# Kernel optimization log

Measured on AMD Instinct MI355X. Metric: run time of the kernel, lower is better.

The kernel has to match this reference:

```python
import jax, jax.numpy as jnp
import numpy as np

B, T, DM = 2, 512, 1024
H, DH = 16, 64          # n_heads, d_head = d_model // n_heads
D, R = 32, 4            # d_manifold, metric_net rank
TEMP_MIN = 0.5


def _rope_tables(t_len, d_head):
    inv_freq = 1.0 / (10000.0 ** (jnp.arange(0, d_head, 2, dtype=jnp.float32) / d_head))
    t = jnp.arange(t_len, dtype=jnp.float32)
    freqs = t[:, None] * inv_freq[None, :]          # [T, d_head//2]
    emb = jnp.concatenate([freqs, freqs], axis=-1)  # [T, d_head]
    return jnp.cos(emb), jnp.sin(emb)


def _apply_rope(x, cos, sin):
    # x: [B, H, T, d_head]
    half = x.shape[-1] // 2
    x1, x2 = x[..., :half], x[..., half:]
    c1 = cos[None, None, :, :half]
    s1 = sin[None, None, :, :half]
    return jnp.concatenate([x1 * c1 - x2 * s1, x1 * s1 + x2 * c1], axis=-1)


def setup_inputs() -> dict:
    key = jax.random.key(0)
    ks = jax.random.split(key, 9)
    s = 0.02
    return {
        "x": jax.random.normal(ks[0], (B, T, DM), dtype=jnp.float32),
        "Wq": s * jax.random.normal(ks[1], (DM, DM), dtype=jnp.float32),
        "Wk": s * jax.random.normal(ks[2], (DM, DM), dtype=jnp.float32),
        "Wv": s * jax.random.normal(ks[3], (DM, DM), dtype=jnp.float32),
        "Wo": s * jax.random.normal(ks[4], (DM, DM), dtype=jnp.float32),
        "Wqm": s * jax.random.normal(ks[5], (DH, D), dtype=jnp.float32),
        "Wkm": s * jax.random.normal(ks[6], (DH, D), dtype=jnp.float32),
        "Wmetric": s * jax.random.normal(ks[7], (D, D * R), dtype=jnp.float32),
        "temperature": jnp.asarray(1.0, dtype=jnp.float32),
    }


def reference(x, Wq, Wk, Wv, Wo, Wqm, Wkm, Wmetric, temperature):
    b, t, c = x.shape
    # projections -> [B, H, T, d_head]
    def split_heads(y):
        return y.reshape(b, t, H, DH).transpose(0, 2, 1, 3)
    q = split_heads(x @ Wq)
    k = split_heads(x @ Wk)
    v = split_heads(x @ Wv)

    cos, sin = _rope_tables(t, DH)
    q = _apply_rope(q, cos, sin)
    k = _apply_rope(k, cos, sin)

    # manifold coordinates in (0,1): [B, H, T, D]
    qm = jax.nn.sigmoid(jnp.einsum('bhtd,dm->bhtm', q, Wqm))
    km = jax.nn.sigmoid(jnp.einsum('bhtd,dm->bhtm', k, Wkm))

    # low-rank metric factor U(q): [B, H, T, D, R]
    U = jnp.einsum('bhtm,mn->bhtn', qm, Wmetric).reshape(b, H, t, D, R)

    # Euclidean part: ||q_i - k_j||^2 = |q|^2 + |k|^2 - 2 q.k  -> [B,H,T,T]
    q2 = jnp.sum(qm * qm, axis=-1)
    k2 = jnp.sum(km * km, axis=-1)
    qk = jnp.einsum('bhid,bhjd->bhij', qm, km)
    dist_euc = q2[..., :, None] + k2[..., None, :] - 2.0 * qk

    # low-rank part: ||U_i^T (q_i - k_j)||^2, factorized as U_i^T q_i - U_i^T k_j
    Uq = jnp.einsum('bhidr,bhid->bhir', U, qm)          # [B,H,T,R]
    Uk = jnp.einsum('bhidr,bhjd->bhijr', U, km)         # [B,H,T,T,R]
    dist_lr = jnp.sum((Uq[:, :, :, None, :] - Uk) ** 2, axis=-1)

    dist_sq = jnp.maximum(dist_euc + dist_lr, 0.0)

    temp = jnp.maximum(temperature, TEMP_MIN)
    attn = -dist_sq / temp

    causal = jnp.triu(jnp.ones((t, t), dtype=bool), k=1)
    attn = jnp.where(causal[None, None], -jnp.inf, attn)
    attn = jax.nn.softmax(attn, axis=-1)

    out = jnp.einsum('bhij,bhjd->bhid', attn, v)        # [B,H,T,d_head]
    out = out.transpose(0, 2, 1, 3).reshape(b, t, c)
    return out @ Wo
```

## Files before the change

kernel.cpp:

```cpp
#include <hip/hip_runtime.h>
#include <cmath>

constexpr int B_  = 2;
constexpr int T_  = 512;
constexpr int DM_ = 1024;
constexpr int H_  = 16;
constexpr int DH_ = 64;
constexpr int D_  = 32;
constexpr int R_  = 4;
constexpr int BH_ = B_ * H_;

typedef __bf16 bf16x8 __attribute__((ext_vector_type(8)));
typedef float  f32x4  __attribute__((ext_vector_type(4)));
typedef unsigned short u16x8 __attribute__((ext_vector_type(8)));

__device__ __forceinline__ unsigned short f2bf(float f) {
    unsigned u = __float_as_uint(f);
    return (unsigned short)((u + 0x7fffu + ((u >> 16) & 1u)) >> 16);
}
__device__ __forceinline__ float bf2f(unsigned short v) {
    return __uint_as_float((unsigned)v << 16);
}
__device__ __forceinline__ void gload16(const void* g, void* l) {
    __builtin_amdgcn_global_load_lds(
        (const __attribute__((address_space(1))) void*)g,
        (__attribute__((address_space(3))) void*)l, 16, 0, 0);
}

__global__ __launch_bounds__(256) void prep_kernel(
    const float* __restrict__ x,
    const float* __restrict__ Wq, const float* __restrict__ Wk,
    const float* __restrict__ Wv, const float* __restrict__ Wo,
    unsigned short* __restrict__ xb,
    unsigned short* __restrict__ wqb, unsigned short* __restrict__ wkb,
    unsigned short* __restrict__ wvb, unsigned short* __restrict__ wob)
{
    const int t = threadIdx.x;
    const int z = blockIdx.z;
    if (z == 4) {
        int base = (blockIdx.y * 16 + blockIdx.x) * 4096 + t * 16;
#pragma unroll
        for (int c = 0; c < 4; ++c) {
            float4 v = *(const float4*)&x[base + c * 4];
            ushort4 o = { f2bf(v.x), f2bf(v.y), f2bf(v.z), f2bf(v.w) };
            *(ushort4*)&xb[base + c * 4] = o;
        }
        return;
    }
    __shared__ __align__(16) unsigned short Ls[64][72];
    const float* W = (z == 0) ? Wq : (z == 1) ? Wk : (z == 2) ? Wv : Wo;
    unsigned short* O = (z == 0) ? wqb : (z == 1) ? wkb : (z == 2) ? wvb : wob;
    const int k0 = blockIdx.x * 64;
    const int n0 = blockIdx.y * 64;
#pragma unroll
    for (int it = 0; it < 4; ++it) {
        int r = it * 16 + (t >> 4);
        int c = (t & 15) * 4;
        float4 v4 = *(const float4*)&W[(size_t)(k0 + r) * DM_ + n0 + c];
        Ls[c + 0][r] = f2bf(v4.x); Ls[c + 1][r] = f2bf(v4.y);
        Ls[c + 2][r] = f2bf(v4.z); Ls[c + 3][r] = f2bf(v4.w);
    }
    __syncthreads();
#pragma unroll
    for (int it = 0; it < 2; ++it) {
        int nl = it * 32 + (t >> 3);
        int kc = (t & 7) * 8;
        *(u16x8*)&O[(size_t)(n0 + nl) * DM_ + k0 + kc] = *(const u16x8*)&Ls[nl][kc];
    }
}

__global__ __launch_bounds__(256) void qkv_feat_gemm(
    const unsigned short* __restrict__ A,
    const unsigned short* __restrict__ wqb, const unsigned short* __restrict__ wkb,
    const unsigned short* __restrict__ wvb,
    const float* __restrict__ Wqm, const float* __restrict__ Wkm,
    const float* __restrict__ Wmetric,
    unsigned short* __restrict__ a_hi, unsigned short* __restrict__ a_lo,
    unsigned short* __restrict__ km_hi, unsigned short* __restrict__ km_lo,
    float* __restrict__ q2p, float* __restrict__ k2,
    unsigned short* __restrict__ Urb, unsigned short* __restrict__ vT)
{
    __shared__ union {
        struct { __align__(16) unsigned short As[64 * 64];
                 __align__(16) unsigned short Bs[64 * 64]; } g;
        struct { float Ct[64][65];
                 float qms[4][32]; float Us[4][128]; float Uqs[4][4]; } f;
    } sh;

    const int tid  = threadIdx.x;
    const int lane = tid & 63;
    const int w    = tid >> 6;
    const int wm   = (w & 1) * 32;
    const int wn   = (w >> 1) * 32;
    const int l15  = lane & 15, quad = lane >> 4;

    const int bm = blockIdx.y * 64;
    const int n0 = blockIdx.x * 64;
    const int which = n0 >> 10;
    const int bn = n0 & 1023;
    const int h  = bn >> 6;
    const unsigned short* Bt = (which == 0) ? wqb : (which == 1) ? wkb : wvb;

    const int srow = tid >> 3, kcs = tid & 7, kcg = kcs ^ (srow & 7);
    const unsigned short* Ap0 = A  + (size_t)(bm + srow) * DM_ + kcg * 8;
    const unsigned short* Bp0 = Bt + (size_t)(bn + srow) * DM_ + kcg * 8;
    const unsigned short* Ap1 = Ap0 + 32 * DM_;
    const unsigned short* Bp1 = Bp0 + 32 * DM_;
    unsigned short* As0 = &sh.g.As[tid * 8];
    unsigned short* Bs0 = &sh.g.Bs[tid * 8];
    unsigned short* As1 = As0 + 2048;
    unsigned short* Bs1 = Bs0 + 2048;

    f32x4 acc[2][2] = {};
    for (int k0 = 0; k0 < DM_; k0 += 64) {
        gload16(Ap0 + k0, As0);
        gload16(Ap1 + k0, As1);
        gload16(Bp0 + k0, Bs0);
        gload16(Bp1 + k0, Bs1);
        __syncthreads();
        bf16x8 af[2][2], bfr[2][2];
#pragma unroll
        for (int ki = 0; ki < 2; ++ki)
#pragma unroll
            for (int i = 0; i < 2; ++i) {
                int ra = wm + i * 16 + l15;
                int rb = wn + i * 16 + l15;
                int kch = ki * 4 + quad;
                af[ki][i]  = *(const bf16x8*)&sh.g.As[ra * 64 + (kch ^ (ra & 7)) * 8];
                bfr[ki][i] = *(const bf16x8*)&sh.g.Bs[rb * 64 + (kch ^ (rb & 7)) * 8];
            }
#pragma unroll
        for (int mi = 0; mi < 2; ++mi)
#pragma unroll
            for (int ni = 0; ni < 2; ++ni) {
                acc[mi][ni] = __builtin_amdgcn_mfma_f32_16x16x32_bf16(
                    af[0][mi], bfr[0][ni], acc[mi][ni], 0, 0, 0);
                acc[mi][ni] = __builtin_amdgcn_mfma_f32_16x16x32_bf16(
                    af[1][mi], bfr[1][ni], acc[mi][ni], 0, 0, 0);
            }
        __syncthreads();
    }

    if (which == 2) {
#pragma unroll
        for (int mi = 0; mi < 2; ++mi)
#pragma unroll
            for (int ni = 0; ni < 2; ++ni) {
                f32x4 a = acc[mi][ni];
                int d = wn + ni * 16 + l15;
#pragma unroll
                for (int r = 0; r < 4; ++r) {
                    int row = bm + wm + mi * 16 + quad * 4 + r;
                    int bb = row >> 9, tt = row & (T_ - 1);
                    vT[(((size_t)bb * H_ + h) * DH_ + d) * T_ + tt] = f2bf(a[r]);
                }
            }
        return;
    }

#pragma unroll
    for (int mi = 0; mi < 2; ++mi)
#pragma unroll
        for (int ni = 0; ni < 2; ++ni) {
            f32x4 a = acc[mi][ni];
            int cl = wn + ni * 16 + l15;
#pragma unroll
            for (int r = 0; r < 4; ++r)
                sh.f.Ct[wm + mi * 16 + quad * 4 + r][cl] = a[r];
        }
    __syncthreads();

    for (int e = tid; e < 2048; e += 256) {
        int row = e >> 5, d = e & 31;
        int t = (bm + row) & (T_ - 1);
        float ang = (float)t * expf((float)d * -0.28782313662425575f);
        float s, c;
        sincosf(ang, &s, &c);
        float v1 = sh.f.Ct[row][d], v2 = sh.f.Ct[row][d + 32];
        sh.f.Ct[row][d]      = v1 * c - v2 * s;
        sh.f.Ct[row][d + 32] = v1 * s + v2 * c;
    }
    __syncthreads();

    const float* Wm = (which == 0) ? Wqm : Wkm;
    for (int rr = w; rr < 64; rr += 4) {
        const int m_ = bm + rr;
        const int b_ = m_ >> 9, t_ = m_ & (T_ - 1);
        const int bh = b_ * H_ + h;
        const size_t rowg = (size_t)bh * T_ + t_;

        float qmv = 0.f;
        if (lane < 32) {
            float acc2 = 0.f;
#pragma unroll 8
            for (int d = 0; d < 64; ++d)
                acc2 += sh.f.Ct[rr][d] * Wm[d * 32 + lane];
            qmv = 1.0f / (1.0f + __expf(-acc2));
            sh.f.qms[w][lane] = qmv;
        }

        if (which == 1) {
            if (lane < 32) {
                unsigned short hv = f2bf(qmv);
                km_hi[rowg * 32 + lane] = hv;
                km_lo[rowg * 32 + lane] = f2bf(qmv - bf2f(hv));
                float p = qmv * qmv;
                p += __shfl_xor(p, 1);  p += __shfl_xor(p, 2);
                p += __shfl_xor(p, 4);  p += __shfl_xor(p, 8);
                p += __shfl_xor(p, 16);
                if (lane == 0) k2[rowg] = p;
            }
            continue;
        }

        float a0 = 0.f, a1 = 0.f;
#pragma unroll 8
        for (int m = 0; m < 32; ++m) {
            float qv = sh.f.qms[w][m];
            a0 += qv * Wmetric[m * 128 + lane];
            a1 += qv * Wmetric[m * 128 + 64 + lane];
        }
        sh.f.Us[w][lane] = a0; sh.f.Us[w][64 + lane] = a1;
        {
            int r0 = lane & 3, d0 = lane >> 2, d1 = 16 + (lane >> 2);
            Urb[(((size_t)bh * R_ + r0) * T_ + t_) * D_ + d0] = f2bf(a0);
            Urb[(((size_t)bh * R_ + r0) * T_ + t_) * D_ + d1] = f2bf(a1);
        }
        if (lane < 4) {
            float acc2 = 0.f;
#pragma unroll
            for (int d = 0; d < 32; ++d)
                acc2 += sh.f.Us[w][d * 4 + lane] * sh.f.qms[w][d];
            sh.f.Uqs[w][lane] = acc2;
        }
        if (lane < 32) {
            float b = sh.f.Uqs[w][0] * sh.f.Us[w][lane * 4 + 0]
                    + sh.f.Uqs[w][1] * sh.f.Us[w][lane * 4 + 1]
                    + sh.f.Uqs[w][2] * sh.f.Us[w][lane * 4 + 2]
                    + sh.f.Uqs[w][3] * sh.f.Us[w][lane * 4 + 3];
            float a = sh.f.qms[w][lane] + b;
            unsigned short hv = f2bf(a);
            a_hi[rowg * 32 + lane] = hv;
            a_lo[rowg * 32 + lane] = f2bf(a - bf2f(hv));
        }
        if (lane == 0) {
            float acc2 = 0.f;
#pragma unroll
            for (int m = 0; m < 32; ++m)
                acc2 += sh.f.qms[w][m] * sh.f.qms[w][m];
#pragma unroll
            for (int r = 0; r < 4; ++r)
                acc2 += sh.f.Uqs[w][r] * sh.f.Uqs[w][r];
            q2p[rowg] = acc2;
        }
    }
}

constexpr int PROW = 40;
__global__ __launch_bounds__(256) void attn_mfma(
    const unsigned short* __restrict__ a_hi, const unsigned short* __restrict__ a_lo,
    const unsigned short* __restrict__ km_hi, const unsigned short* __restrict__ km_lo,
    const unsigned short* __restrict__ Urb,
    const float* __restrict__ q2p, const float* __restrict__ k2,
    const float* __restrict__ temp_p, const unsigned short* __restrict__ vT,
    unsigned short* __restrict__ ctxb)
{
    __shared__ __align__(16) unsigned short P_lds[4][32 * PROW];
    __shared__ __align__(16) float OP[4][32][64];
    __shared__ float ML[4][32];

    const int itile = blockIdx.x, bh = blockIdx.y;
    const int i0 = itile * 32;
    const int tid = threadIdx.x, w = tid >> 6, lane = tid & 63;
    const int l15 = lane & 15, quad = lane >> 4;

    const float inv_temp = 1.0f / fmaxf(temp_p[0], 0.5f);

    bf16x8 Ahi[2], Alo[2], Aur[4][2];
#pragma unroll
    for (int mi = 0; mi < 2; ++mi) {
        size_t ab = ((size_t)bh * T_ + i0 + mi * 16 + l15) * 32 + quad * 8;
        Ahi[mi] = *(const bf16x8*)&a_hi[ab];
        Alo[mi] = *(const bf16x8*)&a_lo[ab];
#pragma unroll
        for (int r = 0; r < 4; ++r)
            Aur[r][mi] = *(const bf16x8*)
                &Urb[(((size_t)bh * R_ + r) * T_ + i0 + mi * 16 + l15) * 32 + quad * 8];
    }
    float q2r[2][4];
#pragma unroll
    for (int mi = 0; mi < 2; ++mi)
#pragma unroll
        for (int rg = 0; rg < 4; ++rg)
            q2r[mi][rg] = q2p[(size_t)bh * T_ + i0 + mi * 16 + quad * 4 + rg];

    f32x4 Oacc[2][4] = {};
    float psum[2][4] = {};

    for (int jt = w; jt <= itile; jt += 4) {
        const int j0 = jt * 32;
        bf16x8 Bhi[2], Blo[2];
#pragma unroll
        for (int ni = 0; ni < 2; ++ni) {
            size_t kb = ((size_t)bh * T_ + j0 + ni * 16 + l15) * 32 + quad * 8;
            Bhi[ni] = *(const bf16x8*)&km_hi[kb];
            Blo[ni] = *(const bf16x8*)&km_lo[kb];
        }
        f32x4 acc[2][2] = {};
#pragma unroll
        for (int mi = 0; mi < 2; ++mi)
#pragma unroll
            for (int ni = 0; ni < 2; ++ni) {
                acc[mi][ni] = __builtin_amdgcn_mfma_f32_16x16x32_bf16(
                    Alo[mi], Bhi[ni], acc[mi][ni], 0, 0, 0);
                acc[mi][ni] = __builtin_amdgcn_mfma_f32_16x16x32_bf16(
                    Ahi[mi], Blo[ni], acc[mi][ni], 0, 0, 0);
                acc[mi][ni] = __builtin_amdgcn_mfma_f32_16x16x32_bf16(
                    Ahi[mi], Bhi[ni], acc[mi][ni], 0, 0, 0);
            }
        f32x4 sq[2][2] = {};
#pragma unroll
        for (int r = 0; r < 4; ++r) {
            f32x4 ar[2][2] = {};
#pragma unroll
            for (int mi = 0; mi < 2; ++mi)
#pragma unroll
                for (int ni = 0; ni < 2; ++ni)
                    ar[mi][ni] = __builtin_amdgcn_mfma_f32_16x16x32_bf16(
                        Aur[r][mi], Bhi[ni], ar[mi][ni], 0, 0, 0);
#pragma unroll
            for (int mi = 0; mi < 2; ++mi)
#pragma unroll
                for (int ni = 0; ni < 2; ++ni)
                    sq[mi][ni] += ar[mi][ni] * ar[mi][ni];
        }
        float k2c[2];
#pragma unroll
        for (int ni = 0; ni < 2; ++ni)
            k2c[ni] = k2[(size_t)bh * T_ + j0 + ni * 16 + l15];
        const bool diag = (jt == itile);
#pragma unroll
        for (int mi = 0; mi < 2; ++mi)
#pragma unroll
            for (int ni = 0; ni < 2; ++ni)
#pragma unroll
                for (int rg = 0; rg < 4; ++rg) {
                    float dist = q2r[mi][rg] + k2c[ni]
                               - 2.f * acc[mi][ni][rg] + sq[mi][ni][rg];
                    float sc = -fmaxf(dist, 0.f) * inv_temp;
                    if (diag && (ni * 16 + l15) > (mi * 16 + quad * 4 + rg))
                        sc = -1e30f;
                    float p = __expf(sc);
                    psum[mi][rg] += p;
                    P_lds[w][(mi * 16 + quad * 4 + rg) * PROW + ni * 16 + l15] = f2bf(p);
                }
        bf16x8 Pf[2], Vf[4];
#pragma unroll
        for (int mi = 0; mi < 2; ++mi)
            Pf[mi] = *(const bf16x8*)&P_lds[w][(mi * 16 + l15) * PROW + quad * 8];
#pragma unroll
        for (int n4 = 0; n4 < 4; ++n4)
            Vf[n4] = *(const bf16x8*)
                &vT[((size_t)bh * DH_ + n4 * 16 + l15) * T_ + j0 + quad * 8];
#pragma unroll
        for (int mi = 0; mi < 2; ++mi)
#pragma unroll
            for (int n4 = 0; n4 < 4; ++n4)
                Oacc[mi][n4] = __builtin_amdgcn_mfma_f32_16x16x32_bf16(
                    Pf[mi], Vf[n4], Oacc[mi][n4], 0, 0, 0);
    }

#pragma unroll
    for (int mi = 0; mi < 2; ++mi)
#pragma unroll
        for (int rg = 0; rg < 4; ++rg) {
            float v = psum[mi][rg];
            v += __shfl_xor(v, 1); v += __shfl_xor(v, 2);
            v += __shfl_xor(v, 4); v += __shfl_xor(v, 8);
            psum[mi][rg] = v;
        }
    if (l15 == 0)
#pragma unroll
        for (int mi = 0; mi < 2; ++mi)
#pragma unroll
            for (int rg = 0; rg < 4; ++rg)
                ML[w][mi * 16 + quad * 4 + rg] = psum[mi][rg];
#pragma unroll
    for (int mi = 0; mi < 2; ++mi)
#pragma unroll
        for (int n4 = 0; n4 < 4; ++n4)
#pragma unroll
            for (int rg = 0; rg < 4; ++rg)
                OP[w][mi * 16 + quad * 4 + rg][n4 * 16 + l15] = Oacc[mi][n4][rg];
    __syncthreads();

    const int ii = tid >> 3, ds = tid & 7;
    float l = ML[0][ii] + ML[1][ii] + ML[2][ii] + ML[3][ii];
    float O[8] = {};
#pragma unroll
    for (int wv = 0; wv < 4; ++wv) {
        float4 o0 = *(const float4*)&OP[wv][ii][ds * 8];
        float4 o1 = *(const float4*)&OP[wv][ii][ds * 8 + 4];
        O[0] += o0.x; O[1] += o0.y; O[2] += o0.z; O[3] += o0.w;
        O[4] += o1.x; O[5] += o1.y; O[6] += o1.z; O[7] += o1.w;
    }
    const float inv = 1.0f / l;
    const int b = bh >> 4, h = bh & 15;
    u16x8 o;
#pragma unroll
    for (int dd = 0; dd < 8; ++dd) o[dd] = f2bf(O[dd] * inv);
    *(u16x8*)&ctxb[((size_t)b * T_ + i0 + ii) * DM_ + h * 64 + ds * 8] = o;
}

__global__ __launch_bounds__(256) void out_gemm_bk64(
    const unsigned short* __restrict__ A, const unsigned short* __restrict__ Bt,
    float* __restrict__ C)
{
    __shared__ __align__(16) unsigned short As[64 * 64];
    __shared__ __align__(16) unsigned short Bs[64 * 64];
    const int tid  = threadIdx.x;
    const int lane = tid & 63;
    const int w    = tid >> 6;
    const int wm   = (w & 1) * 32;
    const int wn   = (w >> 1) * 32;
    const int l15  = lane & 15, quad = lane >> 4;
    const int bm = blockIdx.y * 64;
    const int bn = blockIdx.x * 64;

    const int srow = tid >> 3, kcs = tid & 7, kcg = kcs ^ (srow & 7);
    const unsigned short* Ap0 = A  + (size_t)(bm + srow) * DM_ + kcg * 8;
    const unsigned short* Bp0 = Bt + (size_t)(bn + srow) * DM_ + kcg * 8;
    const unsigned short* Ap1 = Ap0 + 32 * DM_;
    const unsigned short* Bp1 = Bp0 + 32 * DM_;
    unsigned short* As0 = &As[tid * 8];
    unsigned short* Bs0 = &Bs[tid * 8];
    unsigned short* As1 = As0 + 2048;
    unsigned short* Bs1 = Bs0 + 2048;

    f32x4 acc[2][2] = {};
    for (int k0 = 0; k0 < DM_; k0 += 64) {
        gload16(Ap0 + k0, As0);
        gload16(Ap1 + k0, As1);
        gload16(Bp0 + k0, Bs0);
        gload16(Bp1 + k0, Bs1);
        __syncthreads();
        bf16x8 af[2][2], bfr[2][2];
#pragma unroll
        for (int ki = 0; ki < 2; ++ki)
#pragma unroll
            for (int i = 0; i < 2; ++i) {
                int ra = wm + i * 16 + l15;
                int rb = wn + i * 16 + l15;
                int kch = ki * 4 + quad;
                af[ki][i]  = *(const bf16x8*)&As[ra * 64 + (kch ^ (ra & 7)) * 8];
                bfr[ki][i] = *(const bf16x8*)&Bs[rb * 64 + (kch ^ (rb & 7)) * 8];
            }
#pragma unroll
        for (int mi = 0; mi < 2; ++mi)
#pragma unroll
            for (int ni = 0; ni < 2; ++ni) {
                acc[mi][ni] = __builtin_amdgcn_mfma_f32_16x16x32_bf16(
                    af[0][mi], bfr[0][ni], acc[mi][ni], 0, 0, 0);
                acc[mi][ni] = __builtin_amdgcn_mfma_f32_16x16x32_bf16(
                    af[1][mi], bfr[1][ni], acc[mi][ni], 0, 0, 0);
            }
        __syncthreads();
    }
#pragma unroll
    for (int mi = 0; mi < 2; ++mi)
#pragma unroll
        for (int ni = 0; ni < 2; ++ni) {
            f32x4 a = acc[mi][ni];
            int col = bn + wn + ni * 16 + l15;
#pragma unroll
            for (int r = 0; r < 4; ++r) {
                int row = bm + wm + mi * 16 + quad * 4 + r;
                C[(size_t)row * DM_ + col] = a[r];
            }
        }
}

extern "C" void kernel_launch(void* const* d_in, const int* in_sizes, int n_in,
                              void* d_out, int out_size, void* d_ws, size_t ws_size,
                              hipStream_t stream)
{
    const float* x       = (const float*)d_in[0];
    const float* Wq      = (const float*)d_in[1];
    const float* Wk      = (const float*)d_in[2];
    const float* Wv      = (const float*)d_in[3];
    const float* Wo      = (const float*)d_in[4];
    const float* Wqm     = (const float*)d_in[5];
    const float* Wkm     = (const float*)d_in[6];
    const float* Wmetric = (const float*)d_in[7];
    const float* temp    = (const float*)d_in[8];
    float* out = (float*)d_out;
    float* ws  = (float*)d_ws;

    float* q2p = ws;
    float* k2  = q2p + (size_t)BH_ * T_;
    unsigned short* xb   = (unsigned short*)(k2 + (size_t)BH_ * T_);
    unsigned short* wqb  = xb   + (size_t)DM_ * DM_;
    unsigned short* wkb  = wqb  + (size_t)DM_ * DM_;
    unsigned short* wvb  = wkb  + (size_t)DM_ * DM_;
    unsigned short* wob  = wvb  + (size_t)DM_ * DM_;
    unsigned short* a_hi = wob  + (size_t)DM_ * DM_;
    unsigned short* a_lo = a_hi + (size_t)BH_ * T_ * D_;
    unsigned short* kmhi = a_lo + (size_t)BH_ * T_ * D_;
    unsigned short* kmlo = kmhi + (size_t)BH_ * T_ * D_;
    unsigned short* Urb  = kmlo + (size_t)BH_ * T_ * D_;
    unsigned short* vT   = Urb  + (size_t)BH_ * R_ * T_ * D_;
    unsigned short* ctxb = vT   + (size_t)BH_ * DH_ * T_;

    prep_kernel<<<dim3(16, 16, 5), 256, 0, stream>>>(
        x, Wq, Wk, Wv, Wo, xb, wqb, wkb, wvb, wob);
    qkv_feat_gemm<<<dim3(48, 16), 256, 0, stream>>>(
        xb, wqb, wkb, wvb, Wqm, Wkm, Wmetric,
        a_hi, a_lo, kmhi, kmlo, q2p, k2, Urb, vT);
    attn_mfma<<<dim3(T_ / 32, BH_), 256, 0, stream>>>(
        a_hi, a_lo, kmhi, kmlo, Urb, q2p, k2, temp, vT, ctxb);
    out_gemm_bk64<<<dim3(16, 16), 256, 0, stream>>>(ctxb, wob, out);
}
```

Baseline: 159.2 us.

## Fuse all stages into one persistent kernel with grid-wide barriers

Replaces the four separate launches (prep, QKV+feature GEMM, attention, output GEMM) with a single persistent kernel of 512 blocks that loops over work units and separates stages with a software global barrier built on atomics. The feature stage is split out of the QKV GEMM epilogue: raw q/k are written to fp32 workspace and a separate per-row pass applies RoPE, the manifold projections and the metric terms. The aim is to remove launch gaps between kernels. In exchange it adds barrier spin costs, extra global traffic for the raw q/k round trip, and a deadlock risk if the 512 blocks cannot all be resident at once (mitigated only by a timeout).

```diff
diff --git a/kernel.cpp b/kernel.cpp
--- a/kernel.cpp
+++ b/kernel.cpp
@@ -9,6 +9,8 @@
 constexpr int D_  = 32;
 constexpr int R_  = 4;
 constexpr int BH_ = B_ * H_;
+constexpr int PROW = 40;
+constexpr int NBLK = 512;
 
 typedef __bf16 bf16x8 __attribute__((ext_vector_type(8)));
 typedef float  f32x4  __attribute__((ext_vector_type(4)));
@@ -27,121 +29,157 @@
         (__attribute__((address_space(3))) void*)l, 16, 0, 0);
 }
 
-__global__ __launch_bounds__(256) void prep_kernel(
-    const float* __restrict__ x,
-    const float* __restrict__ Wq, const float* __restrict__ Wk,
-    const float* __restrict__ Wv, const float* __restrict__ Wo,
-    unsigned short* __restrict__ xb,
-    unsigned short* __restrict__ wqb, unsigned short* __restrict__ wkb,
-    unsigned short* __restrict__ wvb, unsigned short* __restrict__ wob)
-{
-    const int t = threadIdx.x;
-    const int z = blockIdx.z;
-    if (z == 4) {
-        int base = (blockIdx.y * 16 + blockIdx.x) * 4096 + t * 16;
-#pragma unroll
-        for (int c = 0; c < 4; ++c) {
-            float4 v = *(const float4*)&x[base + c * 4];
-            ushort4 o = { f2bf(v.x), f2bf(v.y), f2bf(v.z), f2bf(v.w) };
-            *(ushort4*)&xb[base + c * 4] = o;
-        }
-        return;
-    }
-    __shared__ __align__(16) unsigned short Ls[64][72];
-    const float* W = (z == 0) ? Wq : (z == 1) ? Wk : (z == 2) ? Wv : Wo;
-    unsigned short* O = (z == 0) ? wqb : (z == 1) ? wkb : (z == 2) ? wvb : wob;
-    const int k0 = blockIdx.x * 64;
-    const int n0 = blockIdx.y * 64;
-#pragma unroll
-    for (int it = 0; it < 4; ++it) {
-        int r = it * 16 + (t >> 4);
-        int c = (t & 15) * 4;
-        float4 v4 = *(const float4*)&W[(size_t)(k0 + r) * DM_ + n0 + c];
-        Ls[c + 0][r] = f2bf(v4.x); Ls[c + 1][r] = f2bf(v4.y);
-        Ls[c + 2][r] = f2bf(v4.z); Ls[c + 3][r] = f2bf(v4.w);
+__device__ __forceinline__ void gsync(int* cnt, int* gen) {
+    __syncthreads();
+    if (threadIdx.x == 0) {
+        __threadfence();
+        int g = __hip_atomic_load(gen, __ATOMIC_RELAXED, __HIP_MEMORY_SCOPE_AGENT);
+        int old = __hip_atomic_fetch_add(cnt, 1, __ATOMIC_ACQ_REL,
+                                         __HIP_MEMORY_SCOPE_AGENT);
+        if (old == NBLK - 1) {
+            __hip_atomic_store(cnt, 0, __ATOMIC_RELAXED, __HIP_MEMORY_SCOPE_AGENT);
+            __hip_atomic_fetch_add(gen, 1, __ATOMIC_RELEASE,
+                                   __HIP_MEMORY_SCOPE_AGENT);
+        } else {
+            long long t0 = clock64();
+            while (__hip_atomic_load(gen, __ATOMIC_ACQUIRE,
+                                     __HIP_MEMORY_SCOPE_AGENT) == g) {
+                if (clock64() - t0 > 50000000LL) break;
+            }
+        }
     }
     __syncthreads();
-#pragma unroll
-    for (int it = 0; it < 2; ++it) {
-        int nl = it * 32 + (t >> 3);
-        int kc = (t & 7) * 8;
-        *(u16x8*)&O[(size_t)(n0 + nl) * DM_ + k0 + kc] = *(const u16x8*)&Ls[nl][kc];
-    }
 }
 
-__global__ __launch_bounds__(256) void qkv_feat_gemm(
-    const unsigned short* __restrict__ A,
-    const unsigned short* __restrict__ wqb, const unsigned short* __restrict__ wkb,
-    const unsigned short* __restrict__ wvb,
-    const float* __restrict__ Wqm, const float* __restrict__ Wkm,
-    const float* __restrict__ Wmetric,
-    unsigned short* __restrict__ a_hi, unsigned short* __restrict__ a_lo,
-    unsigned short* __restrict__ km_hi, unsigned short* __restrict__ km_lo,
-    float* __restrict__ q2p, float* __restrict__ k2,
-    unsigned short* __restrict__ Urb, unsigned short* __restrict__ vT)
+__global__ __launch_bounds__(256, 2) void mega_kernel(
+    const float* __restrict__ x, const float* __restrict__ Wq,
+    const float* __restrict__ Wk, const float* __restrict__ Wv,
+    const float* __restrict__ Wo, const float* __restrict__ Wqm,
+    const float* __restrict__ Wkm, const float* __restrict__ Wmetric,
+    const float* __restrict__ temp_p, float* __restrict__ out,
+    unsigned char* wsb, int* bar)
 {
+    float* q_raw = (float*)wsb;
+    float* k_raw = q_raw + (size_t)BH_ * T_ * DH_;
+    float* q2p   = k_raw + (size_t)BH_ * T_ * DH_;
+    float* k2    = q2p   + (size_t)BH_ * T_;
+    unsigned short* xb   = (unsigned short*)(k2 + (size_t)BH_ * T_);
+    unsigned short* wqb  = xb   + (size_t)DM_ * DM_;
+    unsigned short* wkb  = wqb  + (size_t)DM_ * DM_;
+    unsigned short* wvb  = wkb  + (size_t)DM_ * DM_;
+    unsigned short* wob  = wvb  + (size_t)DM_ * DM_;
+    unsigned short* a_hi = wob  + (size_t)DM_ * DM_;
+    unsigned short* a_lo = a_hi + (size_t)BH_ * T_ * D_;
+    unsigned short* kmhi = a_lo + (size_t)BH_ * T_ * D_;
+    unsigned short* kmlo = kmhi + (size_t)BH_ * T_ * D_;
+    unsigned short* Urb  = kmlo + (size_t)BH_ * T_ * D_;
+    unsigned short* vT   = Urb  + (size_t)BH_ * R_ * T_ * D_;
+    unsigned short* ctxb = vT   + (size_t)BH_ * DH_ * T_;
+    int* bcnt = bar;
+    int* bgen = bar + 1;
+
     __shared__ union {
+        struct { unsigned short Ls[64][72]; } prep;
         struct { __align__(16) unsigned short As[64 * 64];
                  __align__(16) unsigned short Bs[64 * 64]; } g;
-        struct { float Ct[64][65];
-                 float qms[4][32]; float Us[4][128]; float Uqs[4][4]; } f;
+        struct { float qrs[4][64]; float qms[4][32];
+                 float Us[4][128]; float Uqs[4][4]; } f;
+        struct { __align__(16) unsigned short P[4][32 * PROW];
+                 __align__(16) float OP[4][32][64]; float ML[4][32]; } a;
     } sh;
 
+    const int vb   = blockIdx.x;
     const int tid  = threadIdx.x;
     const int lane = tid & 63;
     const int w    = tid >> 6;
-    const int wm   = (w & 1) * 32;
-    const int wn   = (w >> 1) * 32;
     const int l15  = lane & 15, quad = lane >> 4;
 
-    const int bm = blockIdx.y * 64;
-    const int n0 = blockIdx.x * 64;
-    const int which = n0 >> 10;
-    const int bn = n0 & 1023;
-    const int h  = bn >> 6;
-    const unsigned short* Bt = (which == 0) ? wqb : (which == 1) ? wkb : wvb;
-
-    const int srow = tid >> 3, kcs = tid & 7, kcg = kcs ^ (srow & 7);
-    const unsigned short* Ap0 = A  + (size_t)(bm + srow) * DM_ + kcg * 8;
-    const unsigned short* Bp0 = Bt + (size_t)(bn + srow) * DM_ + kcg * 8;
-    const unsigned short* Ap1 = Ap0 + 32 * DM_;
-    const unsigned short* Bp1 = Bp0 + 32 * DM_;
-    unsigned short* As0 = &sh.g.As[tid * 8];
-    unsigned short* Bs0 = &sh.g.Bs[tid * 8];
-    unsigned short* As1 = As0 + 2048;
-    unsigned short* Bs1 = Bs0 + 2048;
-
-    f32x4 acc[2][2] = {};
-    for (int k0 = 0; k0 < DM_; k0 += 64) {
-        gload16(Ap0 + k0, As0);
-        gload16(Ap1 + k0, As1);
-        gload16(Bp0 + k0, Bs0);
-        gload16(Bp1 + k0, Bs1);
+    for (int u = vb; u < 1280; u += NBLK) {
+        const int z = u >> 8, idx = u & 255;
+        if (z == 4) {
+            int base = idx * 4096 + tid * 16;
+#pragma unroll
+            for (int c = 0; c < 4; ++c) {
+                float4 v = *(const float4*)&x[base + c * 4];
+                ushort4 o = { f2bf(v.x), f2bf(v.y), f2bf(v.z), f2bf(v.w) };
+                *(ushort4*)&xb[base + c * 4] = o;
+            }
+        } else {
+            const float* W = (z == 0) ? Wq : (z == 1) ? Wk : (z == 2) ? Wv : Wo;
+            unsigned short* O = (z == 0) ? wqb : (z == 1) ? wkb
+                              : (z == 2) ? wvb : wob;
+            const int k0 = (idx & 15) * 64;
+            const int n0 = (idx >> 4) * 64;
+            __syncthreads();
+#pragma unroll
+            for (int it = 0; it < 4; ++it) {
+                int r = it * 16 + (tid >> 4);
+                int c = (tid & 15) * 4;
+                float4 v4 = *(const float4*)&W[(size_t)(k0 + r) * DM_ + n0 + c];
+                sh.prep.Ls[c + 0][r] = f2bf(v4.x); sh.prep.Ls[c + 1][r] = f2bf(v4.y);
+                sh.prep.Ls[c + 2][r] = f2bf(v4.z); sh.prep.Ls[c + 3][r] = f2bf(v4.w);
+            }
+            __syncthreads();
+#pragma unroll
+            for (int it = 0; it < 2; ++it) {
+                int nl = it * 32 + (tid >> 3);
+                int kc = (tid & 7) * 8;
+                *(u16x8*)&O[(size_t)(n0 + nl) * DM_ + k0 + kc] =
+                    *(const u16x8*)&sh.prep.Ls[nl][kc];
+            }
+        }
+    }
+    gsync(bcnt, bgen);
+
+    for (int u = vb; u < 768; u += NBLK) {
+        const int bm = (u / 48) * 64;
+        const int n0 = (u % 48) * 64;
+        const int which = n0 >> 10;
+        const int bn = n0 & 1023;
+        const unsigned short* Bt = (which == 0) ? wqb : (which == 1) ? wkb : wvb;
+
+        const int srow = tid >> 3, kcs = tid & 7, kcg = kcs ^ (srow & 7);
+        const unsigned short* Ap0 = xb + (size_t)(bm + srow) * DM_ + kcg * 8;
+        const unsigned short* Bp0 = Bt + (size_t)(bn + srow) * DM_ + kcg * 8;
+        const unsigned short* Ap1 = Ap0 + 32 * DM_;
+        const unsigned short* Bp1 = Bp0 + 32 * DM_;
+        unsigned short* As0 = &sh.g.As[tid * 8];
+        unsigned short* Bs0 = &sh.g.Bs[tid * 8];
+        unsigned short* As1 = As0 + 2048;
+        unsigned short* Bs1 = Bs0 + 2048;
+        const int wm = (w & 1) * 32, wn = (w >> 1) * 32;
+
+        f32x4 acc[2][2] = {};
         __syncthreads();
-        bf16x8 af[2][2], bfr[2][2];
-#pragma unroll
-        for (int ki = 0; ki < 2; ++ki)
-#pragma unroll
-            for (int i = 0; i < 2; ++i) {
-                int ra = wm + i * 16 + l15;
-                int rb = wn + i * 16 + l15;
-                int kch = ki * 4 + quad;
-                af[ki][i]  = *(const bf16x8*)&sh.g.As[ra * 64 + (kch ^ (ra & 7)) * 8];
-                bfr[ki][i] = *(const bf16x8*)&sh.g.Bs[rb * 64 + (kch ^ (rb & 7)) * 8];
-            }
-#pragma unroll
-        for (int mi = 0; mi < 2; ++mi)
-#pragma unroll
-            for (int ni = 0; ni < 2; ++ni) {
-                acc[mi][ni] = __builtin_amdgcn_mfma_f32_16x16x32_bf16(
-                    af[0][mi], bfr[0][ni], acc[mi][ni], 0, 0, 0);
-                acc[mi][ni] = __builtin_amdgcn_mfma_f32_16x16x32_bf16(
-                    af[1][mi], bfr[1][ni], acc[mi][ni], 0, 0, 0);
-            }
-        __syncthreads();
-    }
-
-    if (which == 2) {
+        for (int k0 = 0; k0 < DM_; k0 += 64) {
+            gload16(Ap0 + k0, As0);
+            gload16(Ap1 + k0, As1);
+            gload16(Bp0 + k0, Bs0);
+            gload16(Bp1 + k0, Bs1);
+            __syncthreads();
+            bf16x8 af[2][2], bfr[2][2];
+#pragma unroll
+            for (int ki = 0; ki < 2; ++ki)
+#pragma unroll
+                for (int i = 0; i < 2; ++i) {
+                    int ra = wm + i * 16 + l15;
+                    int rb = wn + i * 16 + l15;
+                    int kch = ki * 4 + quad;
+                    af[ki][i]  = *(const bf16x8*)&sh.g.As[ra * 64 + (kch ^ (ra & 7)) * 8];
+                    bfr[ki][i] = *(const bf16x8*)&sh.g.Bs[rb * 64 + (kch ^ (rb & 7)) * 8];
+                }
+#pragma unroll
+            for (int mi = 0; mi < 2; ++mi)
+#pragma unroll
+                for (int ni = 0; ni < 2; ++ni) {
+                    acc[mi][ni] = __builtin_amdgcn_mfma_f32_16x16x32_bf16(
+                        af[0][mi], bfr[0][ni], acc[mi][ni], 0, 0, 0);
+                    acc[mi][ni] = __builtin_amdgcn_mfma_f32_16x16x32_bf16(
+                        af[1][mi], bfr[1][ni], acc[mi][ni], 0, 0, 0);
+                }
+            __syncthreads();
+        }
+        const int h = bn >> 6;
 #pragma unroll
         for (int mi = 0; mi < 2; ++mi)
 #pragma unroll
@@ -152,332 +190,307 @@
                 for (int r = 0; r < 4; ++r) {
                     int row = bm + wm + mi * 16 + quad * 4 + r;
                     int bb = row >> 9, tt = row & (T_ - 1);
-                    vT[(((size_t)bb * H_ + h) * DH_ + d) * T_ + tt] = f2bf(a[r]);
-                }
-            }
-        return;
+                    if (which == 2) {
+                        vT[(((size_t)bb * H_ + h) * DH_ + d) * T_ + tt] = f2bf(a[r]);
+                    } else {
+                        float* C = (which == 0) ? q_raw : k_raw;
+                        C[(((size_t)bb * H_ + h) * T_ + tt) * DH_ + d] = a[r];
+                    }
+                }
+            }
     }
-
-#pragma unroll
-    for (int mi = 0; mi < 2; ++mi)
-#pragma unroll
-        for (int ni = 0; ni < 2; ++ni) {
-            f32x4 a = acc[mi][ni];
-            int cl = wn + ni * 16 + l15;
-#pragma unroll
-            for (int r = 0; r < 4; ++r)
-                sh.f.Ct[wm + mi * 16 + quad * 4 + r][cl] = a[r];
-        }
-    __syncthreads();
-
-    for (int e = tid; e < 2048; e += 256) {
-        int row = e >> 5, d = e & 31;
-        int t = (bm + row) & (T_ - 1);
-        float ang = (float)t * expf((float)d * -0.28782313662425575f);
+    gsync(bcnt, bgen);
+
+    for (int u = vb; u < 8192; u += NBLK) {
+        const int side = u & 1;
+        const int row  = (u >> 1) * 4 + w;
+        const int t    = row & (T_ - 1);
+        const int bh   = row >> 9;
+        const float* raw = side ? k_raw : q_raw;
+        const float* Wm  = side ? Wkm   : Wqm;
+
+        float rv = raw[(size_t)row * 64 + lane];
+        int   fi = lane & 31;
+        float ang = (float)t * expf((float)fi * -0.28782313662425575f);
         float s, c;
         sincosf(ang, &s, &c);
-        float v1 = sh.f.Ct[row][d], v2 = sh.f.Ct[row][d + 32];
-        sh.f.Ct[row][d]      = v1 * c - v2 * s;
-        sh.f.Ct[row][d + 32] = v1 * s + v2 * c;
+        float partner = __shfl_xor(rv, 32);
+        float qr = (lane < 32) ? (rv * c - partner * s) : (partner * s + rv * c);
+        sh.f.qrs[w][lane] = qr;
+        __syncthreads();
+
+        if (lane < 32) {
+            float acc = 0.f;
+#pragma unroll 8
+            for (int d = 0; d < 64; ++d) acc += sh.f.qrs[w][d] * Wm[d * 32 + lane];
+            sh.f.qms[w][lane] = 1.0f / (1.0f + __expf(-acc));
+        }
+        __syncthreads();
+
+        if (side == 0) {
+            float a0 = 0.f, a1 = 0.f;
+#pragma unroll 8
+            for (int m = 0; m < 32; ++m) {
+                float qv = sh.f.qms[w][m];
+                a0 += qv * Wmetric[m * 128 + lane];
+                a1 += qv * Wmetric[m * 128 + 64 + lane];
+            }
+            sh.f.Us[w][lane] = a0; sh.f.Us[w][64 + lane] = a1;
+            {
+                int r0 = lane & 3, d0 = lane >> 2;
+                int d1 = 16 + (lane >> 2);
+                Urb[(((size_t)bh * R_ + r0) * T_ + t) * D_ + d0] = f2bf(a0);
+                Urb[(((size_t)bh * R_ + r0) * T_ + t) * D_ + d1] = f2bf(a1);
+            }
+            __syncthreads();
+            if (lane < 4) {
+                float acc = 0.f;
+#pragma unroll
+                for (int d = 0; d < 32; ++d)
+                    acc += sh.f.Us[w][d * 4 + lane] * sh.f.qms[w][d];
+                sh.f.Uqs[w][lane] = acc;
+            }
+            __syncthreads();
+            if (lane < 32) {
+                float b = sh.f.Uqs[w][0] * sh.f.Us[w][lane * 4 + 0]
+                        + sh.f.Uqs[w][1] * sh.f.Us[w][lane * 4 + 1]
+                        + sh.f.Uqs[w][2] * sh.f.Us[w][lane * 4 + 2]
+                        + sh.f.Uqs[w][3] * sh.f.Us[w][lane * 4 + 3];
+                float a = sh.f.qms[w][lane] + b;
+                unsigned short hi = f2bf(a);
+                unsigned short lo = f2bf(a - bf2f(hi));
+                size_t off = (size_t)row * 32 + lane;
+                a_hi[off] = hi; a_lo[off] = lo;
+            }
+            if (lane == 0) {
+                float acc = 0.f;
+#pragma unroll
+                for (int m = 0; m < 32; ++m)
+                    acc += sh.f.qms[w][m] * sh.f.qms[w][m];
+#pragma unroll
+                for (int r = 0; r < 4; ++r)
+                    acc += sh.f.Uqs[w][r] * sh.f.Uqs[w][r];
+                q2p[row] = acc;
+            }
+            __syncthreads();
+        } else {
+            if (lane < 32) {
+                float v = sh.f.qms[w][lane];
+                unsigned short hi = f2bf(v);
+                unsigned short lo = f2bf(v - bf2f(hi));
+                size_t off = (size_t)row * 32 + lane;
+                kmhi[off] = hi; kmlo[off] = lo;
+            }
+            if (lane == 0) {
+                float acc = 0.f;
+#pragma unroll
+                for (int m = 0; m < 32; ++m)
+                    acc += sh.f.qms[w][m] * sh.f.qms[w][m];
+                k2[row] = acc;
+            }
+            __syncthreads();
+        }
     }
-    __syncthreads();
-
-    const float* Wm = (which == 0) ? Wqm : Wkm;
-    for (int rr = w; rr < 64; rr += 4) {
-        const int m_ = bm + rr;
-        const int b_ = m_ >> 9, t_ = m_ & (T_ - 1);
-        const int bh = b_ * H_ + h;
-        const size_t rowg = (size_t)bh * T_ + t_;
-
-        float qmv = 0.f;
-        if (lane < 32) {
-            float acc2 = 0.f;
-#pragma unroll 8
-            for (int d = 0; d < 64; ++d)
-                acc2 += sh.f.Ct[rr][d] * Wm[d * 32 + lane];
-            qmv = 1.0f / (1.0f + __expf(-acc2));
-            sh.f.qms[w][lane] = qmv;
-        }
-
-        if (which == 1) {
-            if (lane < 32) {
-                unsigned short hv = f2bf(qmv);
-                km_hi[rowg * 32 + lane] = hv;
-                km_lo[rowg * 32 + lane] = f2bf(qmv - bf2f(hv));
-                float p = qmv * qmv;
-                p += __shfl_xor(p, 1);  p += __shfl_xor(p, 2);
-                p += __shfl_xor(p, 4);  p += __shfl_xor(p, 8);
-                p += __shfl_xor(p, 16);
-                if (lane == 0) k2[rowg] = p;
-            }
-            continue;
-        }
-
-        float a0 = 0.f, a1 = 0.f;
-#pragma unroll 8
-        for (int m = 0; m < 32; ++m) {
-            float qv = sh.f.qms[w][m];
-            a0 += qv * Wmetric[m * 128 + lane];
-            a1 += qv * Wmetric[m * 128 + 64 + lane];
-        }
-        sh.f.Us[w][lane] = a0; sh.f.Us[w][64 + lane] = a1;
-        {
-            int r0 = lane & 3, d0 = lane >> 2, d1 = 16 + (lane >> 2);
-            Urb[(((size_t)bh * R_ + r0) * T_ + t_) * D_ + d0] = f2bf(a0);
-            Urb[(((size_t)bh * R_ + r0) * T_ + t_) * D_ + d1] = f2bf(a1);
-        }
-        if (lane < 4) {
-            float acc2 = 0.f;
-#pragma unroll
-            for (int d = 0; d < 32; ++d)
-                acc2 += sh.f.Us[w][d * 4 + lane] * sh.f.qms[w][d];
-            sh.f.Uqs[w][lane] = acc2;
-        }
-        if (lane < 32) {
-            float b = sh.f.Uqs[w][0] * sh.f.Us[w][lane * 4 + 0]
-                    + sh.f.Uqs[w][1] * sh.f.Us[w][lane * 4 + 1]
-                    + sh.f.Uqs[w][2] * sh.f.Us[w][lane * 4 + 2]
-                    + sh.f.Uqs[w][3] * sh.f.Us[w][lane * 4 + 3];
-            float a = sh.f.qms[w][lane] + b;
-            unsigned short hv = f2bf(a);
-            a_hi[rowg * 32 + lane] = hv;
-            a_lo[rowg * 32 + lane] = f2bf(a - bf2f(hv));
-        }
-        if (lane == 0) {
-            float acc2 = 0.f;
-#pragma unroll
-            for (int m = 0; m < 32; ++m)
-                acc2 += sh.f.qms[w][m] * sh.f.qms[w][m];
+    gsync(bcnt, bgen);
+
+    {
+        const int itile = vb >> 5, bh = vb & 31;
+        const int i0 = itile * 32;
+        const float inv_temp = 1.0f / fmaxf(temp_p[0], 0.5f);
+
+        bf16x8 Ahi[2], Alo[2], Aur[4][2];
+#pragma unroll
+        for (int mi = 0; mi < 2; ++mi) {
+            size_t ab = ((size_t)bh * T_ + i0 + mi * 16 + l15) * 32 + quad * 8;
+            Ahi[mi] = *(const bf16x8*)&a_hi[ab];
+            Alo[mi] = *(const bf16x8*)&a_lo[ab];
 #pragma unroll
             for (int r = 0; r < 4; ++r)
-                acc2 += sh.f.Uqs[w][r] * sh.f.Uqs[w][r];
-            q2p[rowg] = acc2;
-        }
+                Aur[r][mi] = *(const bf16x8*)
+                    &Urb[(((size_t)bh * R_ + r) * T_ + i0 + mi * 16 + l15) * 32 + quad * 8];
+        }
+        float q2r[2][4];
+#pragma unroll
+        for (int mi = 0; mi < 2; ++mi)
+#pragma unroll
+            for (int rg = 0; rg < 4; ++rg)
+                q2r[mi][rg] = q2p[(size_t)bh * T_ + i0 + mi * 16 + quad * 4 + rg];
+
+        f32x4 Oacc[2][4] = {};
+        float psum[2][4] = {};
+
+        for (int jt = w; jt <= itile; jt += 4) {
+            const int j0 = jt * 32;
+            bf16x8 Bhi[2], Blo[2];
+#pragma unroll
+            for (int ni = 0; ni < 2; ++ni) {
+                size_t kb = ((size_t)bh * T_ + j0 + ni * 16 + l15) * 32 + quad * 8;
+                Bhi[ni] = *(const bf16x8*)&kmhi[kb];
+                Blo[ni] = *(const bf16x8*)&kmlo[kb];
+            }
+            f32x4 acc[2][2] = {};
+#pragma unroll
+            for (int mi = 0; mi < 2; ++mi)
+#pragma unroll
+                for (int ni = 0; ni < 2; ++ni) {
+                    acc[mi][ni] = __builtin_amdgcn_mfma_f32_16x16x32_bf16(
+                        Alo[mi], Bhi[ni], acc[mi][ni], 0, 0, 0);
+                    acc[mi][ni] = __builtin_amdgcn_mfma_f32_16x16x32_bf16(
+                        Ahi[mi], Blo[ni], acc[mi][ni], 0, 0, 0);
+                    acc[mi][ni] = __builtin_amdgcn_mfma_f32_16x16x32_bf16(
+                        Ahi[mi], Bhi[ni], acc[mi][ni], 0, 0, 0);
+                }
+            f32x4 sq[2][2] = {};
+#pragma unroll
+            for (int r = 0; r < 4; ++r) {
+                f32x4 ar[2][2] = {};
+#pragma unroll
+                for (int mi = 0; mi < 2; ++mi)
+#pragma unroll
+                    for (int ni = 0; ni < 2; ++ni)
+                        ar[mi][ni] = __builtin_amdgcn_mfma_f32_16x16x32_bf16(
+                            Aur[r][mi], Bhi[ni], ar[mi][ni], 0, 0, 0);
+#pragma unroll
+                for (int mi = 0; mi < 2; ++mi)
+#pragma unroll
+                    for (int ni = 0; ni < 2; ++ni)
+                        sq[mi][ni] += ar[mi][ni] * ar[mi][ni];
+            }
+            float k2c[2];
+#pragma unroll
+            for (int ni = 0; ni < 2; ++ni)
+                k2c[ni] = k2[(size_t)bh * T_ + j0 + ni * 16 + l15];
+            const bool diag = (jt == itile);
+#pragma unroll
+            for (int mi = 0; mi < 2; ++mi)
+#pragma unroll
+                for (int ni = 0; ni < 2; ++ni)
+#pragma unroll
+                    for (int rg = 0; rg < 4; ++rg) {
+                        float dist = q2r[mi][rg] + k2c[ni]
+                                   - 2.f * acc[mi][ni][rg] + sq[mi][ni][rg];
+                        float sc = -fmaxf(dist, 0.f) * inv_temp;
+                        if (diag && (ni * 16 + l15) > (mi * 16 + quad * 4 + rg))
+                            sc = -1e30f;
+                        float p = __expf(sc);
+                        psum[mi][rg] += p;
+                        sh.a.P[w][(mi * 16 + quad * 4 + rg) * PROW + ni * 16 + l15] = f2bf(p);
+                    }
+            bf16x8 Pf[2], Vf[4];
+#pragma unroll
+            for (int mi = 0; mi < 2; ++mi)
+                Pf[mi] = *(const bf16x8*)&sh.a.P[w][(mi * 16 + l15) * PROW + quad * 8];
+#pragma unroll
+            for (int n4 = 0; n4 < 4; ++n4)
+                Vf[n4] = *(const bf16x8*)
+                    &vT[((size_t)bh * DH_ + n4 * 16 + l15) * T_ + j0 + quad * 8];
+#pragma unroll
+            for (int mi = 0; mi < 2; ++mi)
+#pragma unroll
+                for (int n4 = 0; n4 < 4; ++n4)
+                    Oacc[mi][n4] = __builtin_amdgcn_mfma_f32_16x16x32_bf16(
+                        Pf[mi], Vf[n4], Oacc[mi][n4], 0, 0, 0);
+        }
+
+#pragma unroll
+        for (int mi = 0; mi < 2; ++mi)
+#pragma unroll
+            for (int rg = 0; rg < 4; ++rg) {
+                float v = psum[mi][rg];
+                v += __shfl_xor(v, 1); v += __shfl_xor(v, 2);
+                v += __shfl_xor(v, 4); v += __shfl_xor(v, 8);
+                psum[mi][rg] = v;
+            }
+        if (l15 == 0)
+#pragma unroll
+            for (int mi = 0; mi < 2; ++mi)
+#pragma unroll
+                for (int rg = 0; rg < 4; ++rg)
+                    sh.a.ML[w][mi * 16 + quad * 4 + rg] = psum[mi][rg];
+#pragma unroll
+        for (int mi = 0; mi < 2; ++mi)
+#pragma unroll
+            for (int n4 = 0; n4 < 4; ++n4)
+#pragma unroll
+                for (int rg = 0; rg < 4; ++rg)
+                    sh.a.OP[w][mi * 16 + quad * 4 + rg][n4 * 16 + l15] = Oacc[mi][n4][rg];
+        __syncthreads();
+
+        const int ii = tid >> 3, ds = tid & 7;
+        float l = sh.a.ML[0][ii] + sh.a.ML[1][ii] + sh.a.ML[2][ii] + sh.a.ML[3][ii];
+        float O[8] = {};
+#pragma unroll
+        for (int wv = 0; wv < 4; ++wv) {
+            float4 o0 = *(const float4*)&sh.a.OP[wv][ii][ds * 8];
+            float4 o1 = *(const float4*)&sh.a.OP[wv][ii][ds * 8 + 4];
+            O[0] += o0.x; O[1] += o0.y; O[2] += o0.z; O[3] += o0.w;
+            O[4] += o1.x; O[5] += o1.y; O[6] += o1.z; O[7] += o1.w;
+        }
+        const float inv = 1.0f / l;
+        const int b = bh >> 4, h = bh & 15;
+        u16x8 o;
+#pragma unroll
+        for (int dd = 0; dd < 8; ++dd) o[dd] = f2bf(O[dd] * inv);
+        *(u16x8*)&ctxb[((size_t)b * T_ + i0 + ii) * DM_ + h * 64 + ds * 8] = o;
     }
-}
-
-constexpr int PROW = 40;
-__global__ __launch_bounds__(256) void attn_mfma(
-    const unsigned short* __restrict__ a_hi, const unsigned short* __restrict__ a_lo,
-    const unsigned short* __restrict__ km_hi, const unsigned short* __restrict__ km_lo,
-    const unsigned short* __restrict__ Urb,
-    const float* __restrict__ q2p, const float* __restrict__ k2,
-    const float* __restrict__ temp_p, const unsigned short* __restrict__ vT,
-    unsigned short* __restrict__ ctxb)
-{
-    __shared__ __align__(16) unsigned short P_lds[4][32 * PROW];
-    __shared__ __align__(16) float OP[4][32][64];
-    __shared__ float ML[4][32];
-
-    const int itile = blockIdx.x, bh = blockIdx.y;
-    const int i0 = itile * 32;
-    const int tid = threadIdx.x, w = tid >> 6, lane = tid & 63;
-    const int l15 = lane & 15, quad = lane >> 4;
-
-    const float inv_temp = 1.0f / fmaxf(temp_p[0], 0.5f);
-
-    bf16x8 Ahi[2], Alo[2], Aur[4][2];
-#pragma unroll
-    for (int mi = 0; mi < 2; ++mi) {
-        size_t ab = ((size_t)bh * T_ + i0 + mi * 16 + l15) * 32 + quad * 8;
-        Ahi[mi] = *(const bf16x8*)&a_hi[ab];
-        Alo[mi] = *(const bf16x8*)&a_lo[ab];
-#pragma unroll
-        for (int r = 0; r < 4; ++r)
-            Aur[r][mi] = *(const bf16x8*)
-                &Urb[(((size_t)bh * R_ + r) * T_ + i0 + mi * 16 + l15) * 32 + quad * 8];
+    gsync(bcnt, bgen);
+
+    if (vb < 256) {
+        const int bm = (vb >> 4) * 64;
+        const int bn = (vb & 15) * 64;
+        const int srow = tid >> 3, kcs = tid & 7, kcg = kcs ^ (srow & 7);
+        const unsigned short* Ap0 = ctxb + (size_t)(bm + srow) * DM_ + kcg * 8;
+        const unsigned short* Bp0 = wob  + (size_t)(bn + srow) * DM_ + kcg * 8;
+        const unsigned short* Ap1 = Ap0 + 32 * DM_;
+        const unsigned short* Bp1 = Bp0 + 32 * DM_;
+        unsigned short* As0 = &sh.g.As[tid * 8];
+        unsigned short* Bs0 = &sh.g.Bs[tid * 8];
+        unsigned short* As1 = As0 + 2048;
+        unsigned short* Bs1 = Bs0 + 2048;
+        const int wm = (w & 1) * 32, wn = (w >> 1) * 32;
+
+        f32x4 acc[2][2] = {};
+        for (int k0 = 0; k0 < DM_; k0 += 64) {
+            gload16(Ap0 + k0, As0);
+            gload16(Ap1 + k0, As1);
+            gload16(Bp0 + k0, Bs0);
+            gload16(Bp1 + k0, Bs1);
+            __syncthreads();
+            bf16x8 af[2][2], bfr[2][2];
+#pragma unroll
+            for (int ki = 0; ki < 2; ++ki)
+#pragma unroll
+                for (int i = 0; i < 2; ++i) {
+                    int ra = wm + i * 16 + l15;
+                    int rb = wn + i * 16 + l15;
+                    int kch = ki * 4 + quad;
+                    af[ki][i]  = *(const bf16x8*)&sh.g.As[ra * 64 + (kch ^ (ra & 7)) * 8];
+                    bfr[ki][i] = *(const bf16x8*)&sh.g.Bs[rb * 64 + (kch ^ (rb & 7)) * 8];
+                }
+#pragma unroll
+            for (int mi = 0; mi < 2; ++mi)
+#pragma unroll
+                for (int ni = 0; ni < 2; ++ni) {
+                    acc[mi][ni] = __builtin_amdgcn_mfma_f32_16x16x32_bf16(
+                        af[0][mi], bfr[0][ni], acc[mi][ni], 0, 0, 0);
+                    acc[mi][ni] = __builtin_amdgcn_mfma_f32_16x16x32_bf16(
+                        af[1][mi], bfr[1][ni], acc[mi][ni], 0, 0, 0);
+                }
+            __syncthreads();
+        }
+#pragma unroll
+        for (int mi = 0; mi < 2; ++mi)
+#pragma unroll
+            for (int ni = 0; ni < 2; ++ni) {
+                f32x4 a = acc[mi][ni];
+                int col = bn + wn + ni * 16 + l15;
+#pragma unroll
+                for (int r = 0; r < 4; ++r) {
+                    int row = bm + wm + mi * 16 + quad * 4 + r;
+                    out[(size_t)row * DM_ + col] = a[r];
+                }
+            }
     }
-    float q2r[2][4];
-#pragma unroll
-    for (int mi = 0; mi < 2; ++mi)
-#pragma unroll
-        for (int rg = 0; rg < 4; ++rg)
-            q2r[mi][rg] = q2p[(size_t)bh * T_ + i0 + mi * 16 + quad * 4 + rg];
-
-    f32x4 Oacc[2][4] = {};
-    float psum[2][4] = {};
-
-    for (int jt = w; jt <= itile; jt += 4) {
-        const int j0 = jt * 32;
-        bf16x8 Bhi[2], Blo[2];
-#pragma unroll
-        for (int ni = 0; ni < 2; ++ni) {
-            size_t kb = ((size_t)bh * T_ + j0 + ni * 16 + l15) * 32 + quad * 8;
-            Bhi[ni] = *(const bf16x8*)&km_hi[kb];
-            Blo[ni] = *(const bf16x8*)&km_lo[kb];
-        }
-        f32x4 acc[2][2] = {};
-#pragma unroll
-        for (int mi = 0; mi < 2; ++mi)
-#pragma unroll
-            for (int ni = 0; ni < 2; ++ni) {
-                acc[mi][ni] = __builtin_amdgcn_mfma_f32_16x16x32_bf16(
-                    Alo[mi], Bhi[ni], acc[mi][ni], 0, 0, 0);
-                acc[mi][ni] = __builtin_amdgcn_mfma_f32_16x16x32_bf16(
-                    Ahi[mi], Blo[ni], acc[mi][ni], 0, 0, 0);
-                acc[mi][ni] = __builtin_amdgcn_mfma_f32_16x16x32_bf16(
-                    Ahi[mi], Bhi[ni], acc[mi][ni], 0, 0, 0);
-            }
-        f32x4 sq[2][2] = {};
-#pragma unroll
-        for (int r = 0; r < 4; ++r) {
-            f32x4 ar[2][2] = {};
-#pragma unroll
-            for (int mi = 0; mi < 2; ++mi)
-#pragma unroll
-                for (int ni = 0; ni < 2; ++ni)
-                    ar[mi][ni] = __builtin_amdgcn_mfma_f32_16x16x32_bf16(
-                        Aur[r][mi], Bhi[ni], ar[mi][ni], 0, 0, 0);
-#pragma unroll
-            for (int mi = 0; mi < 2; ++mi)
-#pragma unroll
-                for (int ni = 0; ni < 2; ++ni)
-                    sq[mi][ni] += ar[mi][ni] * ar[mi][ni];
-        }
-        float k2c[2];
-#pragma unroll
-        for (int ni = 0; ni < 2; ++ni)
-            k2c[ni] = k2[(size_t)bh * T_ + j0 + ni * 16 + l15];
-        const bool diag = (jt == itile);
-#pragma unroll
-        for (int mi = 0; mi < 2; ++mi)
-#pragma unroll
-            for (int ni = 0; ni < 2; ++ni)
-#pragma unroll
-                for (int rg = 0; rg < 4; ++rg) {
-                    float dist = q2r[mi][rg] + k2c[ni]
-                               - 2.f * acc[mi][ni][rg] + sq[mi][ni][rg];
-                    float sc = -fmaxf(dist, 0.f) * inv_temp;
-                    if (diag && (ni * 16 + l15) > (mi * 16 + quad * 4 + rg))
-                        sc = -1e30f;
-                    float p = __expf(sc);
-                    psum[mi][rg] += p;
-                    P_lds[w][(mi * 16 + quad * 4 + rg) * PROW + ni * 16 + l15] = f2bf(p);
-                }
-        bf16x8 Pf[2], Vf[4];
-#pragma unroll
-        for (int mi = 0; mi < 2; ++mi)
-            Pf[mi] = *(const bf16x8*)&P_lds[w][(mi * 16 + l15) * PROW + quad * 8];
-#pragma unroll
-        for (int n4 = 0; n4 < 4; ++n4)
-            Vf[n4] = *(const bf16x8*)
-                &vT[((size_t)bh * DH_ + n4 * 16 + l15) * T_ + j0 + quad * 8];
-#pragma unroll
-        for (int mi = 0; mi < 2; ++mi)
-#pragma unroll
-            for (int n4 = 0; n4 < 4; ++n4)
-                Oacc[mi][n4] = __builtin_amdgcn_mfma_f32_16x16x32_bf16(
-                    Pf[mi], Vf[n4], Oacc[mi][n4], 0, 0, 0);
-    }
-
-#pragma unroll
-    for (int mi = 0; mi < 2; ++mi)
-#pragma unroll
-        for (int rg = 0; rg < 4; ++rg) {
-            float v = psum[mi][rg];
-            v += __shfl_xor(v, 1); v += __shfl_xor(v, 2);
-            v += __shfl_xor(v, 4); v += __shfl_xor(v, 8);
-            psum[mi][rg] = v;
-        }
-    if (l15 == 0)
-#pragma unroll
-        for (int mi = 0; mi < 2; ++mi)
-#pragma unroll
-            for (int rg = 0; rg < 4; ++rg)
-                ML[w][mi * 16 + quad * 4 + rg] = psum[mi][rg];
-#pragma unroll
-    for (int mi = 0; mi < 2; ++mi)
-#pragma unroll
-        for (int n4 = 0; n4 < 4; ++n4)
-#pragma unroll
-            for (int rg = 0; rg < 4; ++rg)
-                OP[w][mi * 16 + quad * 4 + rg][n4 * 16 + l15] = Oacc[mi][n4][rg];
-    __syncthreads();
-
-    const int ii = tid >> 3, ds = tid & 7;
-    float l = ML[0][ii] + ML[1][ii] + ML[2][ii] + ML[3][ii];
-    float O[8] = {};
-#pragma unroll
-    for (int wv = 0; wv < 4; ++wv) {
-        float4 o0 = *(const float4*)&OP[wv][ii][ds * 8];
-        float4 o1 = *(const float4*)&OP[wv][ii][ds * 8 + 4];
-        O[0] += o0.x; O[1] += o0.y; O[2] += o0.z; O[3] += o0.w;
-        O[4] += o1.x; O[5] += o1.y; O[6] += o1.z; O[7] += o1.w;
-    }
-    const float inv = 1.0f / l;
-    const int b = bh >> 4, h = bh & 15;
-    u16x8 o;
-#pragma unroll
-    for (int dd = 0; dd < 8; ++dd) o[dd] = f2bf(O[dd] * inv);
-    *(u16x8*)&ctxb[((size_t)b * T_ + i0 + ii) * DM_ + h * 64 + ds * 8] = o;
-}
-
-__global__ __launch_bounds__(256) void out_gemm_bk64(
-    const unsigned short* __restrict__ A, const unsigned short* __restrict__ Bt,
-    float* __restrict__ C)
-{
-    __shared__ __align__(16) unsigned short As[64 * 64];
-    __shared__ __align__(16) unsigned short Bs[64 * 64];
-    const int tid  = threadIdx.x;
-    const int lane = tid & 63;
-    const int w    = tid >> 6;
-    const int wm   = (w & 1) * 32;
-    const int wn   = (w >> 1) * 32;
-    const int l15  = lane & 15, quad = lane >> 4;
-    const int bm = blockIdx.y * 64;
-    const int bn = blockIdx.x * 64;
-
-    const int srow = tid >> 3, kcs = tid & 7, kcg = kcs ^ (srow & 7);
-    const unsigned short* Ap0 = A  + (size_t)(bm + srow) * DM_ + kcg * 8;
-    const unsigned short* Bp0 = Bt + (size_t)(bn + srow) * DM_ + kcg * 8;
-    const unsigned short* Ap1 = Ap0 + 32 * DM_;
-    const unsigned short* Bp1 = Bp0 + 32 * DM_;
-    unsigned short* As0 = &As[tid * 8];
-    unsigned short* Bs0 = &Bs[tid * 8];
-    unsigned short* As1 = As0 + 2048;
-    unsigned short* Bs1 = Bs0 + 2048;
-
-    f32x4 acc[2][2] = {};
-    for (int k0 = 0; k0 < DM_; k0 += 64) {
-        gload16(Ap0 + k0, As0);
-        gload16(Ap1 + k0, As1);
-        gload16(Bp0 + k0, Bs0);
-        gload16(Bp1 + k0, Bs1);
-        __syncthreads();
-        bf16x8 af[2][2], bfr[2][2];
-#pragma unroll
-        for (int ki = 0; ki < 2; ++ki)
-#pragma unroll
-            for (int i = 0; i < 2; ++i) {
-                int ra = wm + i * 16 + l15;
-                int rb = wn + i * 16 + l15;
-                int kch = ki * 4 + quad;
-                af[ki][i]  = *(const bf16x8*)&As[ra * 64 + (kch ^ (ra & 7)) * 8];
-                bfr[ki][i] = *(const bf16x8*)&Bs[rb * 64 + (kch ^ (rb & 7)) * 8];
-            }
-#pragma unroll
-        for (int mi = 0; mi < 2; ++mi)
-#pragma unroll
-            for (int ni = 0; ni < 2; ++ni) {
-                acc[mi][ni] = __builtin_amdgcn_mfma_f32_16x16x32_bf16(
-                    af[0][mi], bfr[0][ni], acc[mi][ni], 0, 0, 0);
-                acc[mi][ni] = __builtin_amdgcn_mfma_f32_16x16x32_bf16(
-                    af[1][mi], bfr[1][ni], acc[mi][ni], 0, 0, 0);
-            }
-        __syncthreads();
-    }
-#pragma unroll
-    for (int mi = 0; mi < 2; ++mi)
-#pragma unroll
-        for (int ni = 0; ni < 2; ++ni) {
-            f32x4 a = acc[mi][ni];
-            int col = bn + wn + ni * 16 + l15;
-#pragma unroll
-            for (int r = 0; r < 4; ++r) {
-                int row = bm + wm + mi * 16 + quad * 4 + r;
-                C[(size_t)row * DM_ + col] = a[r];
-            }
-        }
 }
 
 extern "C" void kernel_launch(void* const* d_in, const int* in_sizes, int n_in,
@@ -494,29 +507,21 @@
     const float* Wmetric = (const float*)d_in[7];
     const float* temp    = (const float*)d_in[8];
     float* out = (float*)d_out;
-    float* ws  = (float*)d_ws;
-
-    float* q2p = ws;
-    float* k2  = q2p + (size_t)BH_ * T_;
+    unsigned char* wsb = (unsigned char*)d_ws;
+
+    float* q_raw = (float*)wsb;
+    float* k_raw = q_raw + (size_t)BH_ * T_ * DH_;
+    float* q2p   = k_raw + (size_t)BH_ * T_ * DH_;
+    float* k2    = q2p   + (size_t)BH_ * T_;
     unsigned short* xb   = (unsigned short*)(k2 + (size_t)BH_ * T_);
-    unsigned short* wqb  = xb   + (size_t)DM_ * DM_;
-    unsigned short* wkb  = wqb  + (size_t)DM_ * DM_;
-    unsigned short* wvb  = wkb  + (size_t)DM_ * DM_;
-    unsigned short* wob  = wvb  + (size_t)DM_ * DM_;
-    unsigned short* a_hi = wob  + (size_t)DM_ * DM_;
-    unsigned short* a_lo = a_hi + (size_t)BH_ * T_ * D_;
-    unsigned short* kmhi = a_lo + (size_t)BH_ * T_ * D_;
-    unsigned short* kmlo = kmhi + (size_t)BH_ * T_ * D_;
-    unsigned short* Urb  = kmlo + (size_t)BH_ * T_ * D_;
-    unsigned short* vT   = Urb  + (size_t)BH_ * R_ * T_ * D_;
-    unsigned short* ctxb = vT   + (size_t)BH_ * DH_ * T_;
-
-    prep_kernel<<<dim3(16, 16, 5), 256, 0, stream>>>(
-        x, Wq, Wk, Wv, Wo, xb, wqb, wkb, wvb, wob);
-    qkv_feat_gemm<<<dim3(48, 16), 256, 0, stream>>>(
-        xb, wqb, wkb, wvb, Wqm, Wkm, Wmetric,
-        a_hi, a_lo, kmhi, kmlo, q2p, k2, Urb, vT);
-    attn_mfma<<<dim3(T_ / 32, BH_), 256, 0, stream>>>(
-        a_hi, a_lo, kmhi, kmlo, Urb, q2p, k2, temp, vT, ctxb);
-    out_gemm_bk64<<<dim3(16, 16), 256, 0, stream>>>(ctxb, wob, out);
+    unsigned short* ctxb = xb
+        + 5 * (size_t)DM_ * DM_
+        + 4 * (size_t)BH_ * T_ * D_
+        + (size_t)BH_ * R_ * T_ * D_
+        + (size_t)BH_ * DH_ * T_;
+    int* bar = (int*)(ctxb + (size_t)BH_ * DH_ * T_);
+
+    hipMemsetAsync(bar, 0, 2 * sizeof(int), stream);
+    mega_kernel<<<dim3(NBLK), dim3(256), 0, stream>>>(
+        x, Wq, Wk, Wv, Wo, Wqm, Wkm, Wmetric, temp, out, wsb, bar);
 }
```

Result: slower. 528.6 us (+232.0%).
